# Optimization experiments

Hardware: AMD Instinct MI355X
Metric: run time of the kernel (lower is better)

Reference implementation:

```python
import jax, jax.numpy as jnp
import numpy as np
from jax import lax

BIG = 1e30  # finite stand-in for +inf to keep grads NaN-free


def _iso_inc(y):
    """Exact non-decreasing isotonic regression (L2) of a 1-D vector via the
    minimax formula: v_i = max_{j<=i} min_{k>=i} mean(y[j..k]).
    Vectorized O(n^2); equivalent to PAVA."""
    n = y.shape[0]
    csum = jnp.concatenate([jnp.zeros((1,), y.dtype), jnp.cumsum(y)])
    j = jnp.arange(n)[:, None]   # row index (block start)
    k = jnp.arange(n)[None, :]   # col index (block end / position i)
    valid = k >= j
    denom = jnp.where(valid, k - j + 1, 1).astype(y.dtype)
    mean = jnp.where(valid, (csum[k + 1] - csum[j]) / denom, BIG)  # [n, n]
    # A[j, i] = min_{k >= i} mean[j, k]
    A = lax.cummin(mean, axis=1, reverse=True)
    # v_i = max_{j <= i} A[j, i]
    B = jnp.where(j <= k, A, -BIG)
    return jnp.max(B, axis=0)


def _iso_dec(y):
    """Non-increasing isotonic regression (what torchsort's isotonic_l2 solves)."""
    return -_iso_inc(-y)


def _soft_rank_l2(x, strength):
    """torchsort.soft_rank with regularization='l2' (Blondel et al. 2020).
    x: [b, n]; rank along last dim. r = s - iso_dec(s - w) un-permuted,
    where s = sort(x/strength, descending) and w = [n, n-1, ..., 1]."""
    n = x.shape[-1]
    theta = x / strength
    perm = jnp.argsort(-theta, axis=-1)                 # descending sort order
    s = jnp.take_along_axis(theta, perm, axis=-1)
    w = jnp.arange(n, 0, -1).astype(x.dtype)            # [n, n-1, ..., 1]
    iso = jax.vmap(_iso_dec)(s - w)
    ret_sorted = s - iso
    inv = jnp.argsort(perm, axis=-1)                    # inverse permutation
    return jnp.take_along_axis(ret_sorted, inv, axis=-1)


def setup_inputs() -> dict:
    key = jax.random.key(0)
    k1, k2 = jax.random.split(key)
    pred = jax.random.normal(k1, (8, 2048), dtype=jnp.float32)
    target = jax.random.normal(k2, (8, 2048), dtype=jnp.float32)
    return {"pred": pred, "target": target}


def reference(pred, target):
    reg_strength = 1.0
    pred_rank = _soft_rank_l2(pred, reg_strength)
    target_rank = _soft_rank_l2(target, reg_strength)
    pc = pred_rank - pred_rank.mean(axis=-1, keepdims=True)
    tc = target_rank - target_rank.mean(axis=-1, keepdims=True)
    covariance = (pc * tc).sum(axis=-1)
    pred_std = jnp.sqrt((pc ** 2).sum(axis=-1))
    target_std = jnp.sqrt((tc ** 2).sum(axis=-1))
    spearman = covariance / (pred_std * target_std + 1e-8)
    return 1.0 - jnp.mean(spearman)
```

## Files before the change

### kernel.cpp

```cpp
#include <hip/hip_runtime.h>
#include <math.h>

#define N      2048
#define B      8
#define NROW   16
#define CHUNKS 32
#define EPB    64
#define K1T    512
#define K2T    512
#define HALF   256
#define EPT    8

typedef unsigned long long u64;
typedef unsigned int       u32;

#define WS_POS 0
#define WS_SV  (NROW * N)

__device__ inline u32 f2key(float f) {
    u32 u = __float_as_uint(f);
    return (u & 0x80000000u) ? ~u : (u | 0x80000000u);
}
__device__ inline float key2f(u32 u) {
    u = (u & 0x80000000u) ? (u & 0x7fffffffu) : ~u;
    return __uint_as_float(u);
}
__device__ inline double wave_red(double v) {
#pragma unroll
    for (int o = 32; o > 0; o >>= 1) v += __shfl_down(v, o, 64);
    return v;
}

__global__ __launch_bounds__(K1T) void count_pos_kernel(
        const float* __restrict__ pred, const float* __restrict__ target,
        int* __restrict__ posg, float* __restrict__ svg,
        float* __restrict__ out) {
    __shared__ u64 keys[N];
    __shared__ u32 scnt[K1T];

    const int t  = threadIdx.x;
    const int rr = blockIdx.x >> 5;
    const int ch = blockIdx.x & 31;
    const float* row = (rr < B) ? pred + (size_t)rr * N
                                : target + (size_t)(rr - B) * N;

    if (blockIdx.x == 0 && t == 0) out[0] = 1.0f;

    {
        const float4 v = *(const float4*)(row + t * 4);
        const int g = t * 4;
        keys[g + 0] = ((u64)f2key(v.x) << 32) | (u32)(g + 0);
        keys[g + 1] = ((u64)f2key(v.y) << 32) | (u32)(g + 1);
        keys[g + 2] = ((u64)f2key(v.z) << 32) | (u32)(g + 2);
        keys[g + 3] = ((u64)f2key(v.w) << 32) | (u32)(g + 3);
    }
    __syncthreads();
    {
        const int e  = t & (EPB - 1);
        const int h  = t >> 6;
        const u64 Ki = keys[ch * EPB + e];
        u32 cnt = 0;
        const int j0 = h * (N / 8);
#pragma unroll 4
        for (int j = j0; j < j0 + N / 8; j += 2) {
            const u64 k0 = keys[j], k1 = keys[j + 1];
            cnt += (k0 > Ki) ? 1u : 0u;
            cnt += (k1 > Ki) ? 1u : 0u;
        }
        scnt[t] = cnt;
    }
    __syncthreads();
    if (t < EPB) {
        u32 p = 0;
#pragma unroll
        for (int k = 0; k < 8; ++k) p += scnt[t + 64 * k];
        const u64 Ki = keys[ch * EPB + t];
        posg[rr * N + ch * EPB + t] = (int)p;
        svg[rr * N + (int)p] = key2f((u32)(Ki >> 32));
    }
}

__global__ __launch_bounds__(K2T) void pava_rank_corr_kernel(
        const float* __restrict__ pred, const float* __restrict__ target,
        const int* __restrict__ posg, const float* __restrict__ svg,
        float* __restrict__ out) {
    __shared__ double bsum[2][N];
    __shared__ int    bcnt[2][N];
    __shared__ int    nb[2][HALF];
    __shared__ int    nf_sh[2];
    __shared__ float  rankt[N];
    __shared__ double red[5][4];

    const int t  = threadIdx.x;
    const int r  = t >> 8;
    const int tt = t & (HALF - 1);
    const int b  = blockIdx.x;
    const int rowid = (r == 0) ? b : b + B;
    const int i0 = tt * EPT;

    const float* svrow = svg + (size_t)rowid * N;
    const float4 sa = *(const float4*)(svrow + i0);
    const float4 sb = *(const float4*)(svrow + i0 + 4);
    const float* row = (r == 0 ? pred : target) + (size_t)b * N;
    const float4 va = *(const float4*)(row + i0);
    const float4 vb = *(const float4*)(row + i0 + 4);
    const int*   pos = posg + (size_t)rowid * N;
    const int4   pa = *(const int4*)(pos + i0);
    const int4   pb = *(const int4*)(pos + i0 + 4);

    {
        const float s8[EPT] = {sa.x, sa.y, sa.z, sa.w, sb.x, sb.y, sb.z, sb.w};
        int m = 0;
#pragma unroll
        for (int e = 0; e < EPT; ++e) {
            const int g = i0 + e;
            double s = (double)s8[e] - (double)(N - g);
            int q = 1;
            while (m > 0) {
                const double ps = bsum[r][i0 + m - 1];
                const int    pq = bcnt[r][i0 + m - 1];
                if (ps * (double)q < s * (double)pq) { s += ps; q += pq; --m; }
                else break;
            }
            bsum[r][i0 + m] = s; bcnt[r][i0 + m] = q; ++m;
        }
        nb[r][tt] = m;
    }

    for (int l = 0; l < 8; ++l) {
        if (l < 2) __syncthreads();
        else       __threadfence_block();
        const int pairs = HALF >> (l + 1);
        if (tt < pairs) {
            const int W  = 1 << l;
            const int c  = tt << (l + 1);
            const int lb = c * EPT;
            const int rb = (c + W) * EPT;
            int m = nb[r][c];
            const int rn = nb[r][c + W];
            for (int x = 0; x < rn; ++x) {
                double s = bsum[r][rb + x]; int q = bcnt[r][rb + x];
                while (m > 0) {
                    const double ps = bsum[r][lb + m - 1];
                    const int    pq = bcnt[r][lb + m - 1];
                    if (ps * (double)q < s * (double)pq) { s += ps; q += pq; --m; }
                    else break;
                }
                bsum[r][lb + m] = s; bcnt[r][lb + m] = q; ++m;
            }
            nb[r][c] = m;
        }
    }

    __threadfence_block();
    if (tt == 0) {
        const int m = nb[r][0];
        float* bm = (float*)&bsum[r][0];
        int st = 0;
        for (int f = 0; f < m; ++f) {
            const int    cq = bcnt[r][f];
            const double s  = bsum[r][f];
            bcnt[r][f] = st;
            bm[f] = (float)(s / (double)cq);
            st += cq;
        }
        nf_sh[r] = m;
    }
    __syncthreads();

    float r8[EPT];
    {
        const float v8[EPT] = {va.x, va.y, va.z, va.w, vb.x, vb.y, vb.z, vb.w};
        const int   p8[EPT] = {pa.x, pa.y, pa.z, pa.w, pb.x, pb.y, pb.z, pb.w};
        const int m = nf_sh[r];
        const float* bm = (const float*)&bsum[r][0];
#pragma unroll
        for (int e = 0; e < EPT; ++e) {
            const int p = p8[e];
            int lo = 0, hi = m - 1;
            while (lo < hi) {
                const int mid = (lo + hi + 1) >> 1;
                if (bcnt[r][mid] <= p) lo = mid; else hi = mid - 1;
            }
            r8[e] = v8[e] - bm[lo];
        }
    }
    if (r == 1) {
#pragma unroll
        for (int e = 0; e < EPT; ++e) rankt[i0 + e] = r8[e];
    }
    __syncthreads();

    if (r == 0) {
        double sp = 0, st = 0, spp = 0, stt = 0, spt = 0;
#pragma unroll
        for (int e = 0; e < EPT; ++e) {
            const double a = (double)r8[e];
            const double c = (double)rankt[i0 + e];
            sp += a; st += c; spp += a * a; stt += c * c; spt += a * c;
        }
        sp  = wave_red(sp);  st  = wave_red(st);
        spp = wave_red(spp); stt = wave_red(stt); spt = wave_red(spt);
        const int w = t >> 6, lane = t & 63;
        if (lane == 0) {
            red[0][w] = sp; red[1][w] = st; red[2][w] = spp;
            red[3][w] = stt; red[4][w] = spt;
        }
    }
    __syncthreads();
    if (t == 0) {
        double a = 0, c = 0, aa = 0, cc = 0, ac = 0;
        for (int i = 0; i < 4; ++i) {
            a += red[0][i]; c += red[1][i]; aa += red[2][i];
            cc += red[3][i]; ac += red[4][i];
        }
        const double n   = (double)N;
        const double cv  = ac - a * c / n;
        const double vp2 = aa - a * a / n;
        const double vt2 = cc - c * c / n;
        const double corr = cv / (sqrt(vp2) * sqrt(vt2) + 1e-8);
        atomicAdd(out, (float)(-corr / (double)B));
    }
}

extern "C" void kernel_launch(void* const* d_in, const int* in_sizes, int n_in,
                              void* d_out, int out_size, void* d_ws, size_t ws_size,
                              hipStream_t stream) {
    const float* pred   = (const float*)d_in[0];
    const float* target = (const float*)d_in[1];
    float* out  = (float*)d_out;
    int*   posg = (int*)d_ws + WS_POS;
    float* svg  = (float*)d_ws + WS_SV;

    count_pos_kernel<<<NROW * CHUNKS, K1T, 0, stream>>>(pred, target, posg, svg, out);
    pava_rank_corr_kernel<<<B, K2T, 0, stream>>>(pred, target, posg, svg, out);
}
```

Before: 21.11 us.

## Scatter sorted values in LDS, store ranks as u16, halve PAVA threads

Kernel 1 no longer writes the sorted values to global memory. It only writes rank positions, now as 16-bit values. Kernel 2 rebuilds the sorted row by scattering the inputs into LDS at those positions. The second kernel also drops from 512 to 256 threads with 16 elements per thread, which removes one merge level and lets one wave per row run the later levels without barriers. This cuts global traffic and scattered global stores, but the sequential per-thread PAVA work doubles and the extra LDS array raises shared-memory use.

```diff
diff --git a/kernel.cpp b/kernel.cpp
--- a/kernel.cpp
+++ b/kernel.cpp
@@ -7,24 +7,18 @@
 #define CHUNKS 32
 #define EPB    64
 #define K1T    512
-#define K2T    512
-#define HALF   256
-#define EPT    8
+#define K2T    256
+#define HALF   128
+#define EPT    16
 
 typedef unsigned long long u64;
 typedef unsigned int       u32;
-
-#define WS_POS 0
-#define WS_SV  (NROW * N)
+typedef unsigned short     u16;
 
 __device__ inline u32 f2key(float f) {
     u32 u = __float_as_uint(f);
     return (u & 0x80000000u) ? ~u : (u | 0x80000000u);
 }
-__device__ inline float key2f(u32 u) {
-    u = (u & 0x80000000u) ? (u & 0x7fffffffu) : ~u;
-    return __uint_as_float(u);
-}
 __device__ inline double wave_red(double v) {
 #pragma unroll
     for (int o = 32; o > 0; o >>= 1) v += __shfl_down(v, o, 64);
@@ -33,8 +27,7 @@
 
 __global__ __launch_bounds__(K1T) void count_pos_kernel(
         const float* __restrict__ pred, const float* __restrict__ target,
-        int* __restrict__ posg, float* __restrict__ svg,
-        float* __restrict__ out) {
+        u16* __restrict__ posg, float* __restrict__ out) {
     __shared__ u64 keys[N];
     __shared__ u32 scnt[K1T];
 
@@ -74,47 +67,60 @@
         u32 p = 0;
 #pragma unroll
         for (int k = 0; k < 8; ++k) p += scnt[t + 64 * k];
-        const u64 Ki = keys[ch * EPB + t];
-        posg[rr * N + ch * EPB + t] = (int)p;
-        svg[rr * N + (int)p] = key2f((u32)(Ki >> 32));
+        posg[rr * N + ch * EPB + t] = (u16)p;
     }
 }
 
 __global__ __launch_bounds__(K2T) void pava_rank_corr_kernel(
         const float* __restrict__ pred, const float* __restrict__ target,
-        const int* __restrict__ posg, const float* __restrict__ svg,
-        float* __restrict__ out) {
+        const u16* __restrict__ posg, float* __restrict__ out) {
+    __shared__ float  sv[2][N];
     __shared__ double bsum[2][N];
     __shared__ int    bcnt[2][N];
     __shared__ int    nb[2][HALF];
     __shared__ int    nf_sh[2];
     __shared__ float  rankt[N];
-    __shared__ double red[5][4];
+    __shared__ double red[5][2];
 
     const int t  = threadIdx.x;
-    const int r  = t >> 8;
+    const int r  = t >> 7;
     const int tt = t & (HALF - 1);
     const int b  = blockIdx.x;
     const int rowid = (r == 0) ? b : b + B;
     const int i0 = tt * EPT;
 
-    const float* svrow = svg + (size_t)rowid * N;
-    const float4 sa = *(const float4*)(svrow + i0);
-    const float4 sb = *(const float4*)(svrow + i0 + 4);
-    const float* row = (r == 0 ? pred : target) + (size_t)b * N;
-    const float4 va = *(const float4*)(row + i0);
-    const float4 vb = *(const float4*)(row + i0 + 4);
-    const int*   pos = posg + (size_t)rowid * N;
-    const int4   pa = *(const int4*)(pos + i0);
-    const int4   pb = *(const int4*)(pos + i0 + 4);
-
-    {
-        const float s8[EPT] = {sa.x, sa.y, sa.z, sa.w, sb.x, sb.y, sb.z, sb.w};
+    float v16[EPT];
+    int   p16[EPT];
+    {
+        const float* row = (r == 0 ? pred : target) + (size_t)b * N;
+#pragma unroll
+        for (int q = 0; q < 4; ++q) {
+            const float4 v = *(const float4*)(row + i0 + q * 4);
+            v16[q * 4 + 0] = v.x; v16[q * 4 + 1] = v.y;
+            v16[q * 4 + 2] = v.z; v16[q * 4 + 3] = v.w;
+        }
+        const uint4* pp = (const uint4*)(posg + (size_t)rowid * N + i0);
+#pragma unroll
+        for (int q = 0; q < 2; ++q) {
+            const uint4 w = pp[q];
+            const u32 ws4[4] = {w.x, w.y, w.z, w.w};
+#pragma unroll
+            for (int k = 0; k < 4; ++k) {
+                p16[q * 8 + 2 * k + 0] = (int)(ws4[k] & 0xffffu);
+                p16[q * 8 + 2 * k + 1] = (int)(ws4[k] >> 16);
+            }
+        }
+#pragma unroll
+        for (int e = 0; e < EPT; ++e) sv[r][p16[e]] = v16[e];
+    }
+    __syncthreads();
+
+    {
         int m = 0;
 #pragma unroll
         for (int e = 0; e < EPT; ++e) {
             const int g = i0 + e;
-            double s = (double)s8[e] - (double)(N - g);
+            double s = (double)sv[r][g] - (double)(N - g);
             int q = 1;
             while (m > 0) {
                 const double ps = bsum[r][i0 + m - 1];
@@ -127,9 +133,9 @@
         nb[r][tt] = m;
     }
 
-    for (int l = 0; l < 8; ++l) {
-        if (l < 2) __syncthreads();
-        else       __threadfence_block();
+    for (int l = 0; l < 7; ++l) {
+        if (l == 0) __syncthreads();
+        else        __threadfence_block();
         const int pairs = HALF >> (l + 1);
         if (tt < pairs) {
             const int W  = 1 << l;
@@ -168,26 +174,24 @@
     }
     __syncthreads();
 
-    float r8[EPT];
-    {
-        const float v8[EPT] = {va.x, va.y, va.z, va.w, vb.x, vb.y, vb.z, vb.w};
-        const int   p8[EPT] = {pa.x, pa.y, pa.z, pa.w, pb.x, pb.y, pb.z, pb.w};
+    float r16[EPT];
+    {
         const int m = nf_sh[r];
         const float* bm = (const float*)&bsum[r][0];
 #pragma unroll
         for (int e = 0; e < EPT; ++e) {
-            const int p = p8[e];
+            const int p = p16[e];
             int lo = 0, hi = m - 1;
             while (lo < hi) {
                 const int mid = (lo + hi + 1) >> 1;
                 if (bcnt[r][mid] <= p) lo = mid; else hi = mid - 1;
             }
-            r8[e] = v8[e] - bm[lo];
+            r16[e] = v16[e] - bm[lo];
         }
     }
     if (r == 1) {
 #pragma unroll
-        for (int e = 0; e < EPT; ++e) rankt[i0 + e] = r8[e];
+        for (int e = 0; e < EPT; ++e) rankt[i0 + e] = r16[e];
     }
     __syncthreads();
 
@@ -195,7 +199,7 @@
         double sp = 0, st = 0, spp = 0, stt = 0, spt = 0;
 #pragma unroll
         for (int e = 0; e < EPT; ++e) {
-            const double a = (double)r8[e];
+            const double a = (double)r16[e];
             const double c = (double)rankt[i0 + e];
             sp += a; st += c; spp += a * a; stt += c * c; spt += a * c;
         }
@@ -210,7 +214,7 @@
     __syncthreads();
     if (t == 0) {
         double a = 0, c = 0, aa = 0, cc = 0, ac = 0;
-        for (int i = 0; i < 4; ++i) {
+        for (int i = 0; i < 2; ++i) {
             a += red[0][i]; c += red[1][i]; aa += red[2][i];
             cc += red[3][i]; ac += red[4][i];
         }
@@ -229,9 +233,8 @@
     const float* pred   = (const float*)d_in[0];
     const float* target = (const float*)d_in[1];
     float* out  = (float*)d_out;
-    int*   posg = (int*)d_ws + WS_POS;
-    float* svg  = (float*)d_ws + WS_SV;
-
-    count_pos_kernel<<<NROW * CHUNKS, K1T, 0, stream>>>(pred, target, posg, svg, out);
-    pava_rank_corr_kernel<<<B, K2T, 0, stream>>>(pred, target, posg, svg, out);
-}
+    u16*   posg = (u16*)d_ws;
+
+    count_pos_kernel<<<NROW * CHUNKS, K1T, 0, stream>>>(pred, target, posg, out);
+    pava_rank_corr_kernel<<<B, K2T, 0, stream>>>(pred, target, posg, out);
+}
```

After: 24.41 us. +15.6%, slower.
